# Optimization experiments

Hardware: AMD Instinct MI355X
Metric: run time of the kernel (lower is better)

The kernel has to match this reference:

```python
import jax, jax.numpy as jnp
import numpy as np

B, T = 64, 1024
RNN_DIM = 256          # lstm input/hidden dim
HID2 = 512             # 2*rnn_hidden_dim (bi-encoder output per char)
POS_DIM = 100
POS_SIZE = 48
LABEL = 96
POS_PAD = 0
APP_ID = 1


def setup_inputs() -> dict:
    key = jax.random.key(0)
    ks = jax.random.split(key, 9)
    s = 0.1
    enc = jax.random.normal(ks[0], (B, T, HID2), jnp.float32)
    pos_id = jax.random.randint(ks[1], (T, B), 0, POS_SIZE)
    start_index = jax.random.randint(ks[2], (T, B), 0, T)
    pos_table = (jax.random.normal(ks[3], (POS_SIZE, POS_DIM), jnp.float32) * s).at[POS_PAD].set(0.0)
    W_ih = jax.random.normal(ks[4], (4 * RNN_DIM, RNN_DIM), jnp.float32) * s
    b_ih = jnp.zeros((4 * RNN_DIM,), jnp.float32)
    W_hh = jax.random.normal(ks[5], (4 * RNN_DIM, RNN_DIM), jnp.float32) * s
    b_hh = jnp.zeros((4 * RNN_DIM,), jnp.float32)
    comb_W = jax.random.normal(ks[6], (RNN_DIM, HID2 + POS_DIM), jnp.float32) * s
    comb_b = jnp.zeros((RNN_DIM,), jnp.float32)
    lin_W = jax.random.normal(ks[7], (LABEL, HID2 + RNN_DIM), jnp.float32) * s
    return {"encoder_out": enc, "pos_table": pos_table, "W_ih": W_ih, "b_ih": b_ih,
            "W_hh": W_hh, "b_hh": b_hh, "comb_W": comb_W, "comb_b": comb_b,
            "lin_W": lin_W, "pos_id": pos_id, "start_index": start_index}


def reference(encoder_out, pos_table, W_ih, b_ih, W_hh, b_hh, comb_W, comb_b, lin_W,
              pos_id, start_index):
    Bn, Tn, D2 = encoder_out.shape
    H = W_hh.shape[1]
    L = lin_W.shape[0]
    dt = encoder_out.dtype
    # prefix sums: P[:, t] = sum of encoder_out[:, :t]  -> [B, T+1, D2]
    P = jnp.concatenate([jnp.zeros((Bn, 1, D2), dt), jnp.cumsum(encoder_out, axis=1)], axis=1)
    # step t consumes decisions made at step t-1 (state.pos_id[-1] / words_startindex[-1])
    prev_pos = jnp.concatenate([jnp.zeros((1, Bn), pos_id.dtype), pos_id[:-1]], axis=0)
    prev_start = jnp.concatenate([jnp.zeros((1, Bn), start_index.dtype), start_index[:-1]], axis=0)
    ts = jnp.arange(Tn)
    enc_t = jnp.swapaxes(encoder_out, 0, 1)   # [T, B, D2]
    P_t = jnp.swapaxes(P[:, :Tn], 0, 1)       # [T, B, D2]; P_t[t] = prefix up to t
    barange = jnp.arange(Bn)
    lab = jnp.arange(L)

    def step(carry, xs):
        h, c = carry
        t, pp, ps, Pt, et = xs
        # variable-length word avg-pool over chars [start, t)  (F.avg_pool1d)
        valid = (ps >= 0) & (t > 0)
        start = jnp.clip(jnp.minimum(ps, t - 1), 0, Tn - 1)
        wsum = Pt - P[barange, start]                       # [B, D2]
        length = jnp.maximum(t - start, 1).astype(dt)
        avg = jnp.where(valid[:, None], wsum / length[:, None], jnp.zeros((), dt))
        pe = pos_table[pp]                                  # [B, pos_dim]
        z = jnp.tanh(jnp.concatenate([pe, avg], axis=1) @ comb_W.T + comb_b)
        z = jnp.where(t > 0, z, jnp.zeros((), dt))          # t==0: z bucket of zeros
        # LSTMCell
        gates = z @ W_ih.T + b_ih + h @ W_hh.T + b_hh
        i_g, f_g, g_g, o_g = jnp.split(gates, 4, axis=1)
        c_new = jax.nn.sigmoid(f_g) * c + jax.nn.sigmoid(i_g) * jnp.tanh(g_g)
        h_new = jax.nn.sigmoid(o_g) * jnp.tanh(c_new)
        # output projection over [h_now, encoder_out[t]]
        out = jnp.concatenate([h_new, et], axis=1) @ lin_W.T
        out = jnp.where((t == 0) & (lab[None, :] == APP_ID), jnp.asarray(-1e10, dt), out)
        return (h_new, c_new), out

    h0 = jnp.zeros((Bn, H), dt)
    (_, _), outs = jax.lax.scan(step, (h0, h0), (ts, prev_pos, prev_start, P_t, enc_t))
    dec = jnp.swapaxes(outs, 0, 1).reshape(Bn * Tn, L)   # cat along dim 1 then view
    return jax.nn.log_softmax(dec, axis=1)
```

## Files before the change

kernel.cpp:

```cpp
#include <hip/hip_runtime.h>

typedef unsigned short u16;
typedef unsigned int u32;
typedef unsigned long long u64;
typedef __attribute__((ext_vector_type(8))) short short8;
typedef __attribute__((ext_vector_type(4))) float f32x4;
typedef __attribute__((ext_vector_type(8))) int i32x8;

#define B_ 64
#define T_ 1024
#define D2_ 512
#define HD_ 256
#define G4_ 1024
#define PD_ 100
#define KX_ 640
#define KO_ 768
#define LBL_ 96
#define LPAD_ 128
#define SCA 125
#define SCB 124

__device__ __forceinline__ float bf2f(u16 u) {
  u32 v = ((u32)u) << 16;
  return __builtin_bit_cast(float, v);
}
__device__ __forceinline__ u16 f2bf(float f) {
  u32 u = __builtin_bit_cast(u32, f);
  u32 r = (u + 0x7fffu + ((u >> 16) & 1u)) >> 16;
  return (u16)r;
}
__device__ __forceinline__ u32 pk2(float a, float b) {
  return (u32)f2bf(a) | ((u32)f2bf(b) << 16);
}
__device__ __forceinline__ float sgm(float x) {
  return __builtin_amdgcn_rcpf(1.f + __builtin_amdgcn_exp2f(-1.442695040888963f * x));
}
__device__ __forceinline__ float thh(float x) {
  return fmaf(-2.f,
              __builtin_amdgcn_rcpf(1.f + __builtin_amdgcn_exp2f(2.885390081777927f * x)),
              1.f);
}
__device__ __forceinline__ u32 enc4(float y) {
  float a = fabsf(y);
  u32 c = 0;
  c = a >= 0.25f ? 1u : c;
  c = a >= 0.75f ? 2u : c;
  c = a >= 1.25f ? 3u : c;
  c = a >= 1.75f ? 4u : c;
  c = a >= 2.5f ? 5u : c;
  c = a >= 3.5f ? 6u : c;
  c = a >= 5.0f ? 7u : c;
  return c | ((__builtin_bit_cast(u32, y) >> 28) & 8u);
}

__global__ __launch_bounds__(256) void k_prep(
    const float* combW, const float* Wih, const float* bih, const float* Whh,
    const float* bhh, const float* linW, u16* wc, u16* wih, u32* w4, u16* wlin,
    float* biasg) {
  int idx = blockIdx.x * 256 + threadIdx.x;
  if (idx < 256 * KX_) {
    int r = idx / KX_, c = idx % KX_;
    wc[idx] = f2bf(c < 612 ? combW[r * 612 + c] : 0.f);
    return;
  }
  idx -= 256 * KX_;
  if (idx < G4_ * HD_) { wih[idx] = f2bf(Wih[idx]); return; }
  idx -= G4_ * HD_;
  if (idx < G4_ * HD_ / 8) {
    int n = idx >> 5, c0 = (idx & 31) * 8;
    const float* wr = Whh + n * 256 + c0;
    u32 word = 0;
#pragma unroll
    for (int i = 0; i < 4; ++i) {
      u32 byte = enc4(wr[2 * i] * 8.f) | (enc4(wr[2 * i + 1] * 8.f) << 4);
      word |= byte << (8 * i);
    }
    w4[n * 32 + (c0 >> 3)] = word;
    return;
  }
  idx -= G4_ * HD_ / 8;
  if (idx < LPAD_ * KO_) {
    int r = idx / KO_;
    wlin[idx] = f2bf(r < LBL_ ? linW[idx] : 0.f);
    return;
  }
  idx -= LPAD_ * KO_;
  if (idx < G4_) biasg[idx] = bih[idx] + bhh[idx];
}

__global__ __launch_bounds__(512) void k_psum(const float* enc, float* S) {
  const int bc = blockIdx.x;
  const int d = threadIdx.x;
  const int b = bc >> 4, c = bc & 15;
  const float* e = enc + (((size_t)b * T_) + c * 64) * D2_ + d;
  float s = 0.f;
#pragma unroll 8
  for (int j = 0; j < 64; ++j) s += e[(size_t)j * D2_];
  S[(size_t)bc * D2_ + d] = s;
}

__global__ __launch_bounds__(512) void k_pwrite(const float* enc, const float* S,
                                                u16* Pb) {
  const int bc = blockIdx.x;
  const int d = threadIdx.x;
  const int b = bc >> 4, c = bc & 15;
  float off = 0.f;
  for (int c2 = 0; c2 < c; ++c2) off += S[((size_t)(b * 16 + c2)) * D2_ + d];
  const float* e = enc + (((size_t)b * T_) + c * 64) * D2_ + d;
  u16* p = Pb + (((size_t)b * T_) + c * 64) * D2_ + d;
#pragma unroll 4
  for (int j = 0; j < 64; ++j) {
    p[(size_t)j * D2_] = f2bf(off);
    off += e[(size_t)j * D2_];
  }
}

__global__ __launch_bounds__(320) void k_xbuild(const u16* Pb, const float* ptab,
                                                const int* pid, const int* sidx,
                                                u16* X) {
  const int tid = threadIdx.x;
  const int row = tid / 80;
  const int ir = tid - row * 80;
  const int m = blockIdx.x * 4 + row;
  const int t = m >> 6, b = m & 63;
  int pp = 0, ps = 0;
  if (t > 0) {
    pp = pid[(t - 1) * B_ + b];
    ps = sidx[(t - 1) * B_ + b];
  }
  bool valid = (ps >= 0) && (t > 0);
  int start = min(ps, t - 1);
  start = max(start, 0);
  start = min(start, T_ - 1);
  float invlen = 1.f / (float)max(t - start, 1);
  const u16* Pt = Pb + ((size_t)b * T_ + t) * D2_;
  const u16* Ps = Pb + ((size_t)b * T_ + start) * D2_;
  const int k0 = ir * 8;
  uint4 o;
  if (k0 >= 104 && k0 + 8 <= 612) {
    if (valid) {
      int d = k0 - 100;
      ushort4 ta = *(const ushort4*)(Pt + d);
      ushort4 tb = *(const ushort4*)(Pt + d + 4);
      ushort4 sa = *(const ushort4*)(Ps + d);
      ushort4 sb = *(const ushort4*)(Ps + d + 4);
      o.x = pk2((bf2f(ta.x) - bf2f(sa.x)) * invlen,
                (bf2f(ta.y) - bf2f(sa.y)) * invlen);
      o.y = pk2((bf2f(ta.z) - bf2f(sa.z)) * invlen,
                (bf2f(ta.w) - bf2f(sa.w)) * invlen);
      o.z = pk2((bf2f(tb.x) - bf2f(sb.x)) * invlen,
                (bf2f(tb.y) - bf2f(sb.y)) * invlen);
      o.w = pk2((bf2f(tb.z) - bf2f(sb.z)) * invlen,
                (bf2f(tb.w) - bf2f(sb.w)) * invlen);
    } else {
      o = (uint4){0, 0, 0, 0};
    }
  } else if (k0 + 8 <= 100) {
    const float* pr = ptab + pp * PD_ + k0;
    o.x = pk2(pr[0], pr[1]);
    o.y = pk2(pr[2], pr[3]);
    o.z = pk2(pr[4], pr[5]);
    o.w = pk2(pr[6], pr[7]);
  } else if (k0 >= 616) {
    o = (uint4){0, 0, 0, 0};
  } else {
    u32 ow[4];
#pragma unroll
    for (int j2 = 0; j2 < 4; ++j2) {
      float v[2];
#pragma unroll
      for (int jj = 0; jj < 2; ++jj) {
        int k = k0 + j2 * 2 + jj;
        float x;
        if (k < PD_) x = ptab[pp * PD_ + k];
        else if (k < 612)
          x = valid ? (bf2f(Pt[k - PD_]) - bf2f(Ps[k - PD_])) * invlen : 0.f;
        else x = 0.f;
        v[jj] = x;
      }
      ow[j2] = pk2(v[0], v[1]);
    }
    o = (uint4){ow[0], ow[1], ow[2], ow[3]};
  }
  *(uint4*)(X + (size_t)m * KX_ + k0) = o;
}

template <int MODE>
__global__ __launch_bounds__(256, 2) void k_gemm(const u16* A, const u16* Bw,
                                                 const float* bias, u16* outb) {
  constexpr int K = (MODE == 0) ? KX_ : HD_;
  constexpr int NOUT = (MODE == 0) ? 256 : 1024;
  __shared__ u16 As[128][40];
  __shared__ u16 Bs[128][40];
  const int m0 = blockIdx.y * 128, n0 = blockIdx.x * 128;
  const int tid = threadIdx.x;
  const int w = tid >> 6, l = tid & 63;
  const int wr = w >> 1, wc = w & 1;
  const int l15 = l & 15, lh = l >> 4;
  const int srow = tid >> 2, sc8 = (tid & 3) * 8;
  int brow0, brow1;
  if constexpr (MODE == 1) {
    int j0 = n0 + srow, j1 = n0 + srow + 64;
    brow0 = (j0 & 3) * 256 + (j0 >> 2);
    brow1 = (j1 & 3) * 256 + (j1 >> 2);
  } else {
    brow0 = n0 + srow;
    brow1 = n0 + srow + 64;
  }
  f32x4 acc[4][4] = {};
  for (int k0 = 0; k0 < K; k0 += 32) {
    uint4 a0 = *(const uint4*)(A + (size_t)(m0 + srow) * K + k0 + sc8);
    uint4 a1 = *(const uint4*)(A + (size_t)(m0 + srow + 64) * K + k0 + sc8);
    uint4 b0 = *(const uint4*)(Bw + (size_t)brow0 * K + k0 + sc8);
    uint4 b1 = *(const uint4*)(Bw + (size_t)brow1 * K + k0 + sc8);
    __syncthreads();
    *(uint4*)&As[srow][sc8] = a0;
    *(uint4*)&As[srow + 64][sc8] = a1;
    *(uint4*)&Bs[srow][sc8] = b0;
    *(uint4*)&Bs[srow + 64][sc8] = b1;
    __syncthreads();
    short8 af[4], bf[4];
#pragma unroll
    for (int i = 0; i < 4; ++i) {
      af[i] = *(const short8*)&As[wr * 64 + i * 16 + l15][lh * 8];
      bf[i] = *(const short8*)&Bs[wc * 64 + i * 16 + l15][lh * 8];
    }
#pragma unroll
    for (int mi = 0; mi < 4; ++mi)
#pragma unroll
      for (int ni = 0; ni < 4; ++ni)
        acc[mi][ni] =
            __builtin_amdgcn_mfma_f32_16x16x32_bf16(af[mi], bf[ni], acc[mi][ni], 0, 0, 0);
  }
#pragma unroll
  for (int mi = 0; mi < 4; ++mi)
#pragma unroll
    for (int ni = 0; ni < 4; ++ni)
#pragma unroll
      for (int r = 0; r < 4; ++r) {
        int gm = m0 + wr * 64 + mi * 16 + lh * 4 + r;
        int gn = n0 + wc * 64 + ni * 16 + l15;
        float v = acc[mi][ni][r];
        if constexpr (MODE == 0) {
          v = tanhf(v + bias[gn]);
          if (gm < 64) v = 0.f;
          outb[(size_t)gm * NOUT + gn] = f2bf(v);
        } else {
          v += bias[(gn & 3) * 256 + (gn >> 2)];
          outb[(size_t)gm * NOUT + gn] = f2bf(v);
        }
      }
}

__global__ __launch_bounds__(512, 2) void k_seq(const u16* G, const u32* w4,
                                                u16* Hout) {
  __shared__ __align__(16) unsigned char hq[2][128];
  const int b = blockIdx.x;
  const int tid = threadIdx.x;
  const int w = tid >> 6, l = tid & 63;
  const int c16 = l & 15, quad = l >> 4;
  const unsigned char* w4b = (const unsigned char*)w4;
  uint4 Bf[2][4][2];
#pragma unroll
  for (int ct = 0; ct < 2; ++ct)
#pragma unroll
    for (int g = 0; g < 4; ++g) {
      int n = g * 256 + w * 32 + ct * 16 + c16;
#pragma unroll
      for (int kb = 0; kb < 2; ++kb)
        Bf[ct][g][kb] = *(const uint4*)(w4b + (size_t)n * 128 + kb * 64 + quad * 16);
    }
  if (tid < 128) hq[0][tid] = 0;
  const int myct = quad >> 1;
  const int mycell = w * 32 + myct * 16 + c16;
  const u16* gptr = G + (size_t)b * 1024 + mycell * 4;
  u64 gq = *(const u64*)gptr;
  float cc = 0.f;
  int cur = 0;
  __syncthreads();
  for (int t = 0; t < T_; ++t) {
    int tn = (t + 1 < T_) ? t + 1 : t;
    u64 ngq = *(const u64*)(gptr + (size_t)tn * 65536);
    uint4 a0 = *(const uint4*)&hq[cur][quad * 16];
    uint4 a1 = *(const uint4*)&hq[cur][64 + quad * 16];
    i32x8 A0 = (i32x8){(int)a0.x, (int)a0.y, (int)a0.z, (int)a0.w, 0, 0, 0, 0};
    i32x8 A1 = (i32x8){(int)a1.x, (int)a1.y, (int)a1.z, (int)a1.w, 0, 0, 0, 0};
    f32x4 acc[2][4];
#pragma unroll
    for (int ct = 0; ct < 2; ++ct)
#pragma unroll
      for (int g = 0; g < 4; ++g) {
        uint4 b0 = Bf[ct][g][0], b1 = Bf[ct][g][1];
        i32x8 B0 = (i32x8){(int)b0.x, (int)b0.y, (int)b0.z, (int)b0.w, 0, 0, 0, 0};
        i32x8 B1 = (i32x8){(int)b1.x, (int)b1.y, (int)b1.z, (int)b1.w, 0, 0, 0, 0};
        f32x4 z4 = (f32x4){0.f, 0.f, 0.f, 0.f};
        z4 = __builtin_amdgcn_mfma_scale_f32_16x16x128_f8f6f4(
            A0, B0, z4, 4, 4, 0, SCA, 0, SCB);
        z4 = __builtin_amdgcn_mfma_scale_f32_16x16x128_f8f6f4(
            A1, B1, z4, 4, 4, 0, SCA, 0, SCB);
        acc[ct][g] = z4;
      }
    bool hi = (myct != 0);
    float vi = (hi ? acc[1][0][0] : acc[0][0][0]) + bf2f((u16)gq);
    float vf = (hi ? acc[1][1][0] : acc[0][1][0]) + bf2f((u16)(gq >> 16));
    float vg = (hi ? acc[1][2][0] : acc[0][2][0]) + bf2f((u16)(gq >> 32));
    float vo = (hi ? acc[1][3][0] : acc[0][3][0]) + bf2f((u16)(gq >> 48));
    cc = sgm(vf) * cc + sgm(vi) * thh(vg);
    float h = sgm(vo) * thh(cc);
    u32 nib = enc4(h * 4.f);
    u32 nib2 = (u32)__shfl_xor((int)nib, 1);
    if ((quad & 1) == 0) {
      if ((c16 & 1) == 0)
        hq[cur ^ 1][mycell >> 1] = (unsigned char)(nib | (nib2 << 4));
      Hout[((size_t)b * 1024 + t) * 256 + mycell] = f2bf(h);
    }
    gq = ngq;
    cur ^= 1;
    __syncthreads();
  }
}

__global__ __launch_bounds__(256) void k_out(const u16* Hs, const float* enc,
                                             const u16* wlin, float* out) {
  __shared__ u16 As[64][40];
  __shared__ u16 Bs[128][40];
  const int m0 = blockIdx.x * 64;
  const int tid = threadIdx.x;
  const int srow = tid >> 2, sc8 = (tid & 3) * 8;
  const int brow = tid >> 1, bc16 = (tid & 1) * 16;
  const int w = tid >> 6, l = tid & 63;
  const int l15 = l & 15, lh = l >> 4;
  f32x4 acc[8] = {};
  for (int k0 = 0; k0 < KO_; k0 += 32) {
    int k = k0 + sc8;
    uint4 av;
    if (k < 256) {
      av = *(const uint4*)(Hs + (size_t)(m0 + srow) * 256 + k);
    } else {
      const float* src = enc + (size_t)(m0 + srow) * 512 + (k - 256);
      float4 f0 = *(const float4*)(src);
      float4 f1 = *(const float4*)(src + 4);
      av.x = pk2(f0.x, f0.y);
      av.y = pk2(f0.z, f0.w);
      av.z = pk2(f1.x, f1.y);
      av.w = pk2(f1.z, f1.w);
    }
    *(uint4*)&As[srow][sc8] = av;
    const u16* bsrc = wlin + (size_t)brow * KO_ + k0 + bc16;
    *(uint4*)&Bs[brow][bc16] = *(const uint4*)(bsrc);
    *(uint4*)&Bs[brow][bc16 + 8] = *(const uint4*)(bsrc + 8);
    __syncthreads();
    short8 a8 = *(const short8*)&As[16 * w + l15][lh * 8];
#pragma unroll
    for (int nt = 0; nt < 8; ++nt) {
      short8 b8 = *(const short8*)&Bs[nt * 16 + l15][lh * 8];
      acc[nt] = __builtin_amdgcn_mfma_f32_16x16x32_bf16(a8, b8, acc[nt], 0, 0, 0);
    }
    __syncthreads();
  }
#pragma unroll
  for (int r = 0; r < 4; ++r) {
    int gm = m0 + 16 * w + lh * 4 + r;
    float v[8];
#pragma unroll
    for (int nt = 0; nt < 8; ++nt) v[nt] = acc[nt][r];
    if ((gm & (T_ - 1)) == 0 && l15 == 1) v[0] = -1e10f;
    float mx = v[0];
#pragma unroll
    for (int nt = 1; nt < 6; ++nt) mx = fmaxf(mx, v[nt]);
#pragma unroll
    for (int s = 1; s < 16; s <<= 1) mx = fmaxf(mx, __shfl_xor(mx, s));
    float s0 = 0.f;
#pragma unroll
    for (int nt = 0; nt < 6; ++nt)
      s0 += __builtin_amdgcn_exp2f(1.442695040888963f * (v[nt] - mx));
#pragma unroll
    for (int s = 1; s < 16; s <<= 1) s0 += __shfl_xor(s0, s);
    float lg = __builtin_amdgcn_logf(s0) * 0.6931471805599453f + mx;
#pragma unroll
    for (int nt = 0; nt < 6; ++nt)
      out[(size_t)gm * LBL_ + nt * 16 + l15] = v[nt] - lg;
  }
}

extern "C" void kernel_launch(void* const* d_in, const int* in_sizes, int n_in,
                              void* d_out, int out_size, void* d_ws, size_t ws_size,
                              hipStream_t stream) {
  const float* enc = (const float*)d_in[0];
  const float* ptab = (const float*)d_in[1];
  const float* Wih = (const float*)d_in[2];
  const float* bih = (const float*)d_in[3];
  const float* Whh = (const float*)d_in[4];
  const float* bhh = (const float*)d_in[5];
  const float* combW = (const float*)d_in[6];
  const float* combb = (const float*)d_in[7];
  const float* linW = (const float*)d_in[8];
  const int* pid = (const int*)d_in[9];
  const int* sidx = (const int*)d_in[10];

  char* ws = (char*)d_ws;
  size_t off = 0;
  auto alloc = [&](size_t bytes) {
    void* p = ws + off;
    off += (bytes + 255) & ~(size_t)255;
    return p;
  };
  void* reg1 = alloc((size_t)B_ * T_ * G4_ * 2);
  u16* Xb = (u16*)alloc((size_t)T_ * B_ * KX_ * 2);
  u16* Z = (u16*)alloc((size_t)T_ * B_ * HD_ * 2);
  u16* wc = (u16*)alloc(256 * KX_ * 2);
  u16* wih = (u16*)alloc(G4_ * HD_ * 2);
  u32* w4 = (u32*)alloc(G4_ * HD_ / 2);
  u16* wlin = (u16*)alloc(LPAD_ * KO_ * 2);
  float* biasg = (float*)alloc(G4_ * 4);
  u16* Pb = (u16*)reg1;
  u16* G = (u16*)reg1;
  u16* Hs = (u16*)Xb;
  float* S = (float*)Z;
  float* out = (float*)d_out;

  k_prep<<<2180, 256, 0, stream>>>(combW, Wih, bih, Whh, bhh, linW, wc, wih, w4,
                                   wlin, biasg);
  k_psum<<<B_ * 16, 512, 0, stream>>>(enc, S);
  k_pwrite<<<B_ * 16, 512, 0, stream>>>(enc, S, Pb);
  k_xbuild<<<T_ * B_ / 4, 320, 0, stream>>>(Pb, ptab, pid, sidx, Xb);
  dim3 g3(2, 512);
  k_gemm<0><<<g3, 256, 0, stream>>>(Xb, wc, combb, Z);
  dim3 g4(8, 512);
  k_gemm<1><<<g4, 256, 0, stream>>>(Z, wih, biasg, G);
  k_seq<<<B_, 512, 0, stream>>>(G, w4, Hs);
  k_out<<<1024, 256, 0, stream>>>(Hs, enc, wlin, out);
}
```

Before: 870.6 us.

## Fuse X-row construction into the combiner GEMM and raise occupancy hints

Removes the separate k_xbuild kernel and its materialized X buffer (T*B*640 bf16). The combiner GEMM now computes the prefix-sum average and position-embedding entries for each A tile on the fly, using per-row metadata staged in shared memory. Launch bounds for the GEMMs and the output kernel rise to 4 blocks per CU. This cuts a global write and re-read of X, but the N=256 GEMM's two column blocks each recompute the same A chunks, and the gather loads are less regular.

```diff
diff --git a/kernel.cpp b/kernel.cpp
--- a/kernel.cpp
+++ b/kernel.cpp
@@ -51,6 +51,51 @@
   c = a >= 3.5f ? 6u : c;
   c = a >= 5.0f ? 7u : c;
   return c | ((__builtin_bit_cast(u32, y) >> 28) & 8u);
+}
+
+__device__ __forceinline__ uint4 xchunk(const u16* Pb, const float* ptab, int pp,
+                                        int rPt, int rPs, float il, int k) {
+  uint4 o;
+  if (k >= 104 && k + 8 <= 612) {
+    const u16* Pt = Pb + (size_t)rPt * D2_ + (k - PD_);
+    const u16* Ps = Pb + (size_t)rPs * D2_ + (k - PD_);
+    ushort4 ta = *(const ushort4*)Pt;
+    ushort4 tb = *(const ushort4*)(Pt + 4);
+    ushort4 sa = *(const ushort4*)Ps;
+    ushort4 sb = *(const ushort4*)(Ps + 4);
+    o.x = pk2((bf2f(ta.x) - bf2f(sa.x)) * il, (bf2f(ta.y) - bf2f(sa.y)) * il);
+    o.y = pk2((bf2f(ta.z) - bf2f(sa.z)) * il, (bf2f(ta.w) - bf2f(sa.w)) * il);
+    o.z = pk2((bf2f(tb.x) - bf2f(sb.x)) * il, (bf2f(tb.y) - bf2f(sb.y)) * il);
+    o.w = pk2((bf2f(tb.z) - bf2f(sb.z)) * il, (bf2f(tb.w) - bf2f(sb.w)) * il);
+  } else if (k + 8 <= 100) {
+    const float* pr = ptab + pp * PD_ + k;
+    o.x = pk2(pr[0], pr[1]);
+    o.y = pk2(pr[2], pr[3]);
+    o.z = pk2(pr[4], pr[5]);
+    o.w = pk2(pr[6], pr[7]);
+  } else if (k >= 616) {
+    o = (uint4){0, 0, 0, 0};
+  } else {
+    u32 ow[4];
+#pragma unroll
+    for (int j2 = 0; j2 < 4; ++j2) {
+      float v[2];
+#pragma unroll
+      for (int jj = 0; jj < 2; ++jj) {
+        int kk = k + j2 * 2 + jj;
+        float x;
+        if (kk < PD_) x = ptab[pp * PD_ + kk];
+        else if (kk < 612)
+          x = (bf2f(Pb[(size_t)rPt * D2_ + kk - PD_]) -
+               bf2f(Pb[(size_t)rPs * D2_ + kk - PD_])) * il;
+        else x = 0.f;
+        v[jj] = x;
+      }
+      ow[j2] = pk2(v[0], v[1]);
+    }
+    o = (uint4){ow[0], ow[1], ow[2], ow[3]};
+  }
+  return o;
 }
 
 __global__ __launch_bounds__(256) void k_prep(
@@ -115,81 +160,86 @@
   }
 }
 
-__global__ __launch_bounds__(320) void k_xbuild(const u16* Pb, const float* ptab,
-                                                const int* pid, const int* sidx,
-                                                u16* X) {
+__global__ __launch_bounds__(256, 4) void k_gemm0(const u16* Pb, const float* ptab,
+                                                  const int* pid, const int* sidx,
+                                                  const u16* Bw, const float* bias,
+                                                  u16* outb) {
+  __shared__ u16 As[128][40];
+  __shared__ u16 Bs[128][40];
+  __shared__ int pp_s[128];
+  __shared__ int pt_s[128];
+  __shared__ int ps_s[128];
+  __shared__ float il_s[128];
+  const int m0 = blockIdx.y * 128, n0 = blockIdx.x * 128;
   const int tid = threadIdx.x;
-  const int row = tid / 80;
-  const int ir = tid - row * 80;
-  const int m = blockIdx.x * 4 + row;
-  const int t = m >> 6, b = m & 63;
-  int pp = 0, ps = 0;
-  if (t > 0) {
-    pp = pid[(t - 1) * B_ + b];
-    ps = sidx[(t - 1) * B_ + b];
-  }
-  bool valid = (ps >= 0) && (t > 0);
-  int start = min(ps, t - 1);
-  start = max(start, 0);
-  start = min(start, T_ - 1);
-  float invlen = 1.f / (float)max(t - start, 1);
-  const u16* Pt = Pb + ((size_t)b * T_ + t) * D2_;
-  const u16* Ps = Pb + ((size_t)b * T_ + start) * D2_;
-  const int k0 = ir * 8;
-  uint4 o;
-  if (k0 >= 104 && k0 + 8 <= 612) {
-    if (valid) {
-      int d = k0 - 100;
-      ushort4 ta = *(const ushort4*)(Pt + d);
-      ushort4 tb = *(const ushort4*)(Pt + d + 4);
-      ushort4 sa = *(const ushort4*)(Ps + d);
-      ushort4 sb = *(const ushort4*)(Ps + d + 4);
-      o.x = pk2((bf2f(ta.x) - bf2f(sa.x)) * invlen,
-                (bf2f(ta.y) - bf2f(sa.y)) * invlen);
-      o.y = pk2((bf2f(ta.z) - bf2f(sa.z)) * invlen,
-                (bf2f(ta.w) - bf2f(sa.w)) * invlen);
-      o.z = pk2((bf2f(tb.x) - bf2f(sb.x)) * invlen,
-                (bf2f(tb.y) - bf2f(sb.y)) * invlen);
-      o.w = pk2((bf2f(tb.z) - bf2f(sb.z)) * invlen,
-                (bf2f(tb.w) - bf2f(sb.w)) * invlen);
-    } else {
-      o = (uint4){0, 0, 0, 0};
-    }
-  } else if (k0 + 8 <= 100) {
-    const float* pr = ptab + pp * PD_ + k0;
-    o.x = pk2(pr[0], pr[1]);
-    o.y = pk2(pr[2], pr[3]);
-    o.z = pk2(pr[4], pr[5]);
-    o.w = pk2(pr[6], pr[7]);
-  } else if (k0 >= 616) {
-    o = (uint4){0, 0, 0, 0};
-  } else {
-    u32 ow[4];
-#pragma unroll
-    for (int j2 = 0; j2 < 4; ++j2) {
-      float v[2];
-#pragma unroll
-      for (int jj = 0; jj < 2; ++jj) {
-        int k = k0 + j2 * 2 + jj;
-        float x;
-        if (k < PD_) x = ptab[pp * PD_ + k];
-        else if (k < 612)
-          x = valid ? (bf2f(Pt[k - PD_]) - bf2f(Ps[k - PD_])) * invlen : 0.f;
-        else x = 0.f;
-        v[jj] = x;
+  const int w = tid >> 6, l = tid & 63;
+  const int wr = w >> 1, wc = w & 1;
+  const int l15 = l & 15, lh = l >> 4;
+  const int srow = tid >> 2, sc8 = (tid & 3) * 8;
+  if (tid < 128) {
+    int m = m0 + tid, t = m >> 6, b = m & 63;
+    int pp = 0, ps = 0;
+    if (t > 0) {
+      pp = pid[(t - 1) * B_ + b];
+      ps = sidx[(t - 1) * B_ + b];
+    }
+    bool valid = (ps >= 0) && (t > 0);
+    int start = min(ps, t - 1);
+    start = max(start, 0);
+    start = min(start, T_ - 1);
+    pp_s[tid] = pp;
+    pt_s[tid] = b * T_ + t;
+    ps_s[tid] = b * T_ + start;
+    il_s[tid] = valid ? 1.f / (float)max(t - start, 1) : 0.f;
+  }
+  __syncthreads();
+  const int r0 = srow, r1 = srow + 64;
+  const int pp0 = pp_s[r0], pt0 = pt_s[r0], psr0 = ps_s[r0];
+  const float il0 = il_s[r0];
+  const int pp1 = pp_s[r1], pt1 = pt_s[r1], psr1 = ps_s[r1];
+  const float il1 = il_s[r1];
+  f32x4 acc[4][4] = {};
+  for (int k0 = 0; k0 < KX_; k0 += 32) {
+    uint4 a0 = xchunk(Pb, ptab, pp0, pt0, psr0, il0, k0 + sc8);
+    uint4 a1 = xchunk(Pb, ptab, pp1, pt1, psr1, il1, k0 + sc8);
+    uint4 b0 = *(const uint4*)(Bw + (size_t)(n0 + srow) * KX_ + k0 + sc8);
+    uint4 b1 = *(const uint4*)(Bw + (size_t)(n0 + srow + 64) * KX_ + k0 + sc8);
+    __syncthreads();
+    *(uint4*)&As[srow][sc8] = a0;
+    *(uint4*)&As[srow + 64][sc8] = a1;
+    *(uint4*)&Bs[srow][sc8] = b0;
+    *(uint4*)&Bs[srow + 64][sc8] = b1;
+    __syncthreads();
+    short8 af[4], bf[4];
+#pragma unroll
+    for (int i = 0; i < 4; ++i) {
+      af[i] = *(const short8*)&As[wr * 64 + i * 16 + l15][lh * 8];
+      bf[i] = *(const short8*)&Bs[wc * 64 + i * 16 + l15][lh * 8];
+    }
+#pragma unroll
+    for (int mi = 0; mi < 4; ++mi)
+#pragma unroll
+      for (int ni = 0; ni < 4; ++ni)
+        acc[mi][ni] =
+            __builtin_amdgcn_mfma_f32_16x16x32_bf16(af[mi], bf[ni], acc[mi][ni], 0, 0, 0);
+  }
+#pragma unroll
+  for (int mi = 0; mi < 4; ++mi)
+#pragma unroll
+    for (int ni = 0; ni < 4; ++ni)
+#pragma unroll
+      for (int r = 0; r < 4; ++r) {
+        int gm = m0 + wr * 64 + mi * 16 + lh * 4 + r;
+        int gn = n0 + wc * 64 + ni * 16 + l15;
+        float v = acc[mi][ni][r];
+        v = tanhf(v + bias[gn]);
+        if (gm < 64) v = 0.f;
+        outb[(size_t)gm * 256 + gn] = f2bf(v);
       }
-      ow[j2] = pk2(v[0], v[1]);
-    }
-    o = (uint4){ow[0], ow[1], ow[2], ow[3]};
-  }
-  *(uint4*)(X + (size_t)m * KX_ + k0) = o;
-}
-
-template <int MODE>
-__global__ __launch_bounds__(256, 2) void k_gemm(const u16* A, const u16* Bw,
-                                                 const float* bias, u16* outb) {
-  constexpr int K = (MODE == 0) ? KX_ : HD_;
-  constexpr int NOUT = (MODE == 0) ? 256 : 1024;
+}
+
+__global__ __launch_bounds__(256, 4) void k_gemm1(const u16* A, const u16* Bw,
+                                                  const float* bias, u16* outb) {
   __shared__ u16 As[128][40];
   __shared__ u16 Bs[128][40];
   const int m0 = blockIdx.y * 128, n0 = blockIdx.x * 128;
@@ -198,21 +248,15 @@
   const int wr = w >> 1, wc = w & 1;
   const int l15 = l & 15, lh = l >> 4;
   const int srow = tid >> 2, sc8 = (tid & 3) * 8;
-  int brow0, brow1;
-  if constexpr (MODE == 1) {
-    int j0 = n0 + srow, j1 = n0 + srow + 64;
-    brow0 = (j0 & 3) * 256 + (j0 >> 2);
-    brow1 = (j1 & 3) * 256 + (j1 >> 2);
-  } else {
-    brow0 = n0 + srow;
-    brow1 = n0 + srow + 64;
-  }
+  int j0 = n0 + srow, j1 = n0 + srow + 64;
+  int brow0 = (j0 & 3) * 256 + (j0 >> 2);
+  int brow1 = (j1 & 3) * 256 + (j1 >> 2);
   f32x4 acc[4][4] = {};
-  for (int k0 = 0; k0 < K; k0 += 32) {
-    uint4 a0 = *(const uint4*)(A + (size_t)(m0 + srow) * K + k0 + sc8);
-    uint4 a1 = *(const uint4*)(A + (size_t)(m0 + srow + 64) * K + k0 + sc8);
-    uint4 b0 = *(const uint4*)(Bw + (size_t)brow0 * K + k0 + sc8);
-    uint4 b1 = *(const uint4*)(Bw + (size_t)brow1 * K + k0 + sc8);
+  for (int k0 = 0; k0 < HD_; k0 += 32) {
+    uint4 a0 = *(const uint4*)(A + (size_t)(m0 + srow) * HD_ + k0 + sc8);
+    uint4 a1 = *(const uint4*)(A + (size_t)(m0 + srow + 64) * HD_ + k0 + sc8);
+    uint4 b0 = *(const uint4*)(Bw + (size_t)brow0 * HD_ + k0 + sc8);
+    uint4 b1 = *(const uint4*)(Bw + (size_t)brow1 * HD_ + k0 + sc8);
     __syncthreads();
     *(uint4*)&As[srow][sc8] = a0;
     *(uint4*)&As[srow + 64][sc8] = a1;
@@ -240,15 +284,8 @@
       for (int r = 0; r < 4; ++r) {
         int gm = m0 + wr * 64 + mi * 16 + lh * 4 + r;
         int gn = n0 + wc * 64 + ni * 16 + l15;
-        float v = acc[mi][ni][r];
-        if constexpr (MODE == 0) {
-          v = tanhf(v + bias[gn]);
-          if (gm < 64) v = 0.f;
-          outb[(size_t)gm * NOUT + gn] = f2bf(v);
-        } else {
-          v += bias[(gn & 3) * 256 + (gn >> 2)];
-          outb[(size_t)gm * NOUT + gn] = f2bf(v);
-        }
+        float v = acc[mi][ni][r] + bias[(gn & 3) * 256 + (gn >> 2)];
+        outb[(size_t)gm * 1024 + gn] = f2bf(v);
       }
 }
 
@@ -320,8 +357,8 @@
   }
 }
 
-__global__ __launch_bounds__(256) void k_out(const u16* Hs, const float* enc,
-                                             const u16* wlin, float* out) {
+__global__ __launch_bounds__(256, 4) void k_out(const u16* Hs, const float* enc,
+                                                const u16* wlin, float* out) {
   __shared__ u16 As[64][40];
   __shared__ u16 Bs[128][40];
   const int m0 = blockIdx.x * 64;
@@ -406,7 +443,7 @@
     return p;
   };
   void* reg1 = alloc((size_t)B_ * T_ * G4_ * 2);
-  u16* Xb = (u16*)alloc((size_t)T_ * B_ * KX_ * 2);
+  u16* Hs = (u16*)alloc((size_t)T_ * B_ * HD_ * 2);
   u16* Z = (u16*)alloc((size_t)T_ * B_ * HD_ * 2);
   u16* wc = (u16*)alloc(256 * KX_ * 2);
   u16* wih = (u16*)alloc(G4_ * HD_ * 2);
@@ -415,7 +452,6 @@
   float* biasg = (float*)alloc(G4_ * 4);
   u16* Pb = (u16*)reg1;
   u16* G = (u16*)reg1;
-  u16* Hs = (u16*)Xb;
   float* S = (float*)Z;
   float* out = (float*)d_out;
 
@@ -423,11 +459,10 @@
                                    wlin, biasg);
   k_psum<<<B_ * 16, 512, 0, stream>>>(enc, S);
   k_pwrite<<<B_ * 16, 512, 0, stream>>>(enc, S, Pb);
-  k_xbuild<<<T_ * B_ / 4, 320, 0, stream>>>(Pb, ptab, pid, sidx, Xb);
   dim3 g3(2, 512);
-  k_gemm<0><<<g3, 256, 0, stream>>>(Xb, wc, combb, Z);
+  k_gemm0<<<g3, 256, 0, stream>>>(Pb, ptab, pid, sidx, wc, combb, Z);
   dim3 g4(8, 512);
-  k_gemm<1><<<g4, 256, 0, stream>>>(Z, wih, biasg, G);
+  k_gemm1<<<g4, 256, 0, stream>>>(Z, wih, biasg, G);
   k_seq<<<B_, 512, 0, stream>>>(G, w4, Hs);
   k_out<<<1024, 256, 0, stream>>>(Hs, enc, wlin, out);
 }
```

Result: no change. 885.7 us (+1.7%).
